# Performance work log

Measured on AMD Instinct MI355X. Metric: run time of the kernel, lower is better.

Reference implementation:

```python
import jax, jax.numpy as jnp
import numpy as np


def setup_inputs() -> dict:
    key = jax.random.key(0)
    k1, k2 = jax.random.split(key)
    B, N, C, H, W = 16, 10000, 3, 32, 32
    x = jax.random.normal(k1, (B, C, H, W), dtype=jnp.float32)
    images = jax.random.normal(k2, (N, C, H, W), dtype=jnp.float32)
    # sval = schedule(t) in (0,1); bt^2 = sval, at = sqrt(1 - sval)
    sval = jnp.asarray(0.5, dtype=jnp.float32)
    return {"x": x, "images": images, "sval": sval}


def reference(x, images, sval):
    # Original math: pwise = x[:,None] - at*images[None]
    #   weights = softmax(-||pwise||^2 / (2 bt^2), over N)
    #   out = -sum_n weights_n * pwise_n / bt^2
    # We decompose ||x - at*img||^2 = ||x||^2 - 2 at x.img + at^2 ||img||^2
    # (GEMM form) and use sum_n w_n (x - at*img_n) = x - at*(w @ imgs),
    # avoiding the [B,N,C,H,W] intermediate. Identical math.
    bt2 = sval                      # bt^2 = schedule(t)
    at = jnp.sqrt(1.0 - sval)       # at = sqrt(1 - schedule(t))
    B = x.shape[0]
    N = images.shape[0]
    xf = x.reshape(B, -1)           # [B, D]
    imf = images.reshape(N, -1)     # [N, D]
    x_sq = jnp.sum(xf * xf, axis=-1)        # [B]
    i_sq = jnp.sum(imf * imf, axis=-1)      # [N]
    cross = xf @ imf.T                      # [B, N]  (main GEMM)
    weight_args = -(x_sq[:, None] - 2.0 * at * cross
                    + (at * at) * i_sq[None, :]) / (2.0 * bt2)
    weights = jax.nn.softmax(weight_args, axis=1)   # [B, N]
    mix = weights @ imf                             # [B, D]
    out = -(xf - at * mix) / bt2                    # [B, D]
    return out.reshape(x.shape)
```

## Files before the change

kernel.cpp:

```cpp
#include <hip/hip_runtime.h>
#include <math.h>

#define BB 16
#define NN 10000
#define DD 3072
#define SEL_CUT 40.0f

#define RSTEP(mm, cc)                                              \
  {                                                                \
    const bool up = (lane & (mm)) != 0;                            \
    _Pragma("unroll")                                              \
    for (int k = 0; k < (cc); ++k) {                               \
      float lo = acc[k], hi = acc[k + (cc)];                       \
      float send = up ? lo : hi;                                   \
      float recv = __shfl_xor(send, (mm), 64);                     \
      acc[k] = (up ? hi : lo) + recv;                              \
    }                                                              \
  }

__global__ __launch_bounds__(256, 3) void k1_partial(
    const float* __restrict__ x, const float* __restrict__ images,
    const float* __restrict__ svalp, float* __restrict__ pd)
{
  const int t = threadIdx.x;
  const int lane = t & 63;
  const int wave = t >> 6;
  const int n0 = blockIdx.x * 16 + wave * 4;
  const int q = blockIdx.y;
  const int d0 = q * 768;

  float acc[64];
  float isq[4];
#pragma unroll
  for (int j = 0; j < 64; ++j) acc[j] = 0.f;
#pragma unroll
  for (int r = 0; r < 4; ++r) isq[r] = 0.f;

#pragma unroll 1
  for (int c = 0; c < 3; ++c) {
    const int dg = d0 + c * 256 + (lane << 2);
    float4 im[4];
#pragma unroll
    for (int r = 0; r < 4; ++r)
      im[r] = *(const float4*)&images[(size_t)(n0 + r) * DD + dg];
#pragma unroll
    for (int r = 0; r < 4; ++r)
      isq[r] += im[r].x * im[r].x + im[r].y * im[r].y +
                im[r].z * im[r].z + im[r].w * im[r].w;
#pragma unroll
    for (int b = 0; b < BB; ++b) {
      float4 xv = *(const float4*)&x[b * DD + dg];
#pragma unroll
      for (int r = 0; r < 4; ++r)
        acc[b * 4 + r] += im[r].x * xv.x + im[r].y * xv.y +
                          im[r].z * xv.z + im[r].w * xv.w;
    }
  }

  RSTEP(32, 32)
  RSTEP(16, 16)
  RSTEP(8, 8)
  RSTEP(4, 4)
  RSTEP(2, 2)
  RSTEP(1, 1)

#pragma unroll
  for (int r = 0; r < 4; ++r) {
    float v = isq[r];
#pragma unroll
    for (int m = 32; m >= 1; m >>= 1) v += __shfl_xor(v, m, 64);
    isq[r] = v;
  }

  const float sval = *svalp;
  const float at = sqrtf(1.f - sval);
  const float c1 = at / sval;
  const float c2 = (1.f - sval) / (2.f * sval);

  const int b = lane >> 2;
  const int r = lane & 3;
  float myisq = isq[0];
  if (r == 1) myisq = isq[1];
  if (r == 2) myisq = isq[2];
  if (r == 3) myisq = isq[3];

  pd[(size_t)b * NN * 4 + (size_t)(n0 + r) * 4 + q] = c1 * acc[0] - c2 * myisq;
}

__global__ __launch_bounds__(1024) void k2_select(
    const float* __restrict__ pd, int* __restrict__ cnt,
    int* __restrict__ idx, float* __restrict__ wv)
{
  __shared__ float red[16];
  __shared__ float mshared, lshared;
  const int b = blockIdx.x;
  const int t = threadIdx.x;
  const int lane = t & 63, wave = t >> 6;
  if (t == 0) cnt[b] = 0;

  float a[10];
#pragma unroll
  for (int i = 0; i < 10; ++i) {
    int n = t + (i << 10);
    if (n < NN) {
      float4 p = *(const float4*)&pd[(size_t)b * NN * 4 + (size_t)n * 4];
      a[i] = (p.x + p.y) + (p.z + p.w);
    } else {
      a[i] = -INFINITY;
    }
  }

  float mx = -INFINITY;
#pragma unroll
  for (int i = 0; i < 10; ++i) mx = fmaxf(mx, a[i]);
#pragma unroll
  for (int m = 32; m >= 1; m >>= 1) mx = fmaxf(mx, __shfl_xor(mx, m, 64));
  if (lane == 0) red[wave] = mx;
  __syncthreads();
  if (wave == 0) {
    float v = (lane < 16) ? red[lane] : -INFINITY;
#pragma unroll
    for (int m = 8; m >= 1; m >>= 1) v = fmaxf(v, __shfl_xor(v, m, 64));
    if (lane == 0) mshared = v;
  }
  __syncthreads();
  mx = mshared;

  float s = 0.f;
#pragma unroll
  for (int i = 0; i < 10; ++i) s += __expf(a[i] - mx);
#pragma unroll
  for (int m = 32; m >= 1; m >>= 1) s += __shfl_xor(s, m, 64);
  if (lane == 0) red[wave] = s;
  __syncthreads();
  if (wave == 0) {
    float v = (lane < 16) ? red[lane] : 0.f;
#pragma unroll
    for (int m = 8; m >= 1; m >>= 1) v += __shfl_xor(v, m, 64);
    if (lane == 0) lshared = v;
  }
  __syncthreads();
  const float invl = 1.f / lshared;

#pragma unroll
  for (int i = 0; i < 10; ++i) {
    if (a[i] > mx - SEL_CUT) {
      int k = atomicAdd(&cnt[b], 1);
      idx[b * NN + k] = t + (i << 10);
      wv[b * NN + k] = __expf(a[i] - mx) * invl;
    }
  }
}

__global__ __launch_bounds__(256) void k3_sparse(
    const float* __restrict__ images, const float* __restrict__ x,
    const float* __restrict__ svalp, const int* __restrict__ cnt,
    const int* __restrict__ idx, const float* __restrict__ wv,
    float* __restrict__ out)
{
  const int b = blockIdx.y;
  const int d0 = blockIdx.x * 1024 + (threadIdx.x << 2);
  const int c = cnt[b];

  float4 acc = make_float4(0.f, 0.f, 0.f, 0.f);
  for (int j = 0; j < c; ++j) {
    int n = idx[b * NN + j];
    float w = wv[b * NN + j];
    float4 im = *(const float4*)&images[(size_t)n * DD + d0];
    acc.x += w * im.x; acc.y += w * im.y;
    acc.z += w * im.z; acc.w += w * im.w;
  }

  const float sval = *svalp;
  const float at = sqrtf(1.f - sval);
  const float inv_bt2 = 1.f / sval;
  float4 xv = *(const float4*)&x[b * DD + d0];
  float4 o;
  o.x = (at * acc.x - xv.x) * inv_bt2;
  o.y = (at * acc.y - xv.y) * inv_bt2;
  o.z = (at * acc.z - xv.z) * inv_bt2;
  o.w = (at * acc.w - xv.w) * inv_bt2;
  *(float4*)&out[b * DD + d0] = o;
}

extern "C" void kernel_launch(void* const* d_in, const int* in_sizes, int n_in,
                              void* d_out, int out_size, void* d_ws, size_t ws_size,
                              hipStream_t stream) {
  const float* x      = (const float*)d_in[0];
  const float* images = (const float*)d_in[1];
  const float* sval   = (const float*)d_in[2];
  float* out = (float*)d_out;
  float* ws  = (float*)d_ws;

  float* pd  = ws;
  int*   cnt = (int*)(ws + 640000);
  int*   idx = (int*)(ws + 640032);
  float* wv  = ws + 800032;

  hipLaunchKernelGGL(k1_partial, dim3(625, 4), dim3(256), 0, stream,
                     x, images, sval, pd);
  hipLaunchKernelGGL(k2_select, dim3(16), dim3(1024), 0, stream,
                     pd, cnt, idx, wv);
  hipLaunchKernelGGL(k3_sparse, dim3(3, 16), dim3(256), 0, stream,
                     images, x, sval, cnt, idx, wv, out);
}
```

Baseline: 235.9 us.

## Keep x slice in registers and stream image pairs with finer D split

The partial-dot kernel now splits D into 12 chunks of 256 and holds the 16 x vectors for its chunk in registers. Each wave loops over 16 images two at a time, prefetching the next pair and reducing the pair dot products with a two-wide shuffle transpose. The partial-sum layout moves to [q][b][n], so the select kernel sums 12 strided partials, and the selected-candidate buffers are capped at 1024 per batch row. The aim is to cut repeated x reloads and the 64-register accumulator, at the cost of more partial writes and reads and more shuffles per image.

```diff
diff --git a/kernel.cpp b/kernel.cpp
--- a/kernel.cpp
+++ b/kernel.cpp
@@ -4,87 +4,100 @@
 #define BB 16
 #define NN 10000
 #define DD 3072
+#define QQ 12
 #define SEL_CUT 40.0f
-
-#define RSTEP(mm, cc)                                              \
-  {                                                                \
-    const bool up = (lane & (mm)) != 0;                            \
-    _Pragma("unroll")                                              \
-    for (int k = 0; k < (cc); ++k) {                               \
-      float lo = acc[k], hi = acc[k + (cc)];                       \
-      float send = up ? lo : hi;                                   \
-      float recv = __shfl_xor(send, (mm), 64);                     \
-      acc[k] = (up ? hi : lo) + recv;                              \
-    }                                                              \
-  }
-
-__global__ __launch_bounds__(256, 3) void k1_partial(
+#define CAP 1024
+
+#define RSTEP2(mm, cc)                                                  \
+  {                                                                     \
+    const bool up = (lane & (mm)) != 0;                                 \
+    _Pragma("unroll")                                                   \
+    for (int k = 0; k < (cc); ++k) {                                    \
+      float2 lo = accp[k], hi = accp[k + (cc)];                         \
+      float sx = up ? lo.x : hi.x, sy = up ? lo.y : hi.y;               \
+      float rx = __shfl_xor(sx, (mm), 64);                              \
+      float ry = __shfl_xor(sy, (mm), 64);                              \
+      accp[k].x = (up ? hi.x : lo.x) + rx;                              \
+      accp[k].y = (up ? hi.y : lo.y) + ry;                              \
+    }                                                                   \
+  }
+
+__global__ __launch_bounds__(256) void k1_partial(
     const float* __restrict__ x, const float* __restrict__ images,
     const float* __restrict__ svalp, float* __restrict__ pd)
 {
   const int t = threadIdx.x;
   const int lane = t & 63;
   const int wave = t >> 6;
-  const int n0 = blockIdx.x * 16 + wave * 4;
   const int q = blockIdx.y;
-  const int d0 = q * 768;
-
-  float acc[64];
-  float isq[4];
-#pragma unroll
-  for (int j = 0; j < 64; ++j) acc[j] = 0.f;
-#pragma unroll
-  for (int r = 0; r < 4; ++r) isq[r] = 0.f;
-
-#pragma unroll 1
-  for (int c = 0; c < 3; ++c) {
-    const int dg = d0 + c * 256 + (lane << 2);
-    float4 im[4];
-#pragma unroll
-    for (int r = 0; r < 4; ++r)
-      im[r] = *(const float4*)&images[(size_t)(n0 + r) * DD + dg];
-#pragma unroll
-    for (int r = 0; r < 4; ++r)
-      isq[r] += im[r].x * im[r].x + im[r].y * im[r].y +
-                im[r].z * im[r].z + im[r].w * im[r].w;
-#pragma unroll
-    for (int b = 0; b < BB; ++b) {
-      float4 xv = *(const float4*)&x[b * DD + dg];
-#pragma unroll
-      for (int r = 0; r < 4; ++r)
-        acc[b * 4 + r] += im[r].x * xv.x + im[r].y * xv.y +
-                          im[r].z * xv.z + im[r].w * xv.w;
-    }
-  }
-
-  RSTEP(32, 32)
-  RSTEP(16, 16)
-  RSTEP(8, 8)
-  RSTEP(4, 4)
-  RSTEP(2, 2)
-  RSTEP(1, 1)
-
-#pragma unroll
-  for (int r = 0; r < 4; ++r) {
-    float v = isq[r];
-#pragma unroll
-    for (int m = 32; m >= 1; m >>= 1) v += __shfl_xor(v, m, 64);
-    isq[r] = v;
-  }
+  const int dg = q * 256 + (lane << 2);
+  const int n0 = (blockIdx.x * 4 + wave) * 16;
+
+  float4 xr[BB];
+#pragma unroll
+  for (int b = 0; b < BB; ++b)
+    xr[b] = *(const float4*)&x[b * DD + dg];
 
   const float sval = *svalp;
   const float at = sqrtf(1.f - sval);
-  const float c1 = at / sval;
-  const float c2 = (1.f - sval) / (2.f * sval);
-
-  const int b = lane >> 2;
-  const int r = lane & 3;
-  float myisq = isq[0];
-  if (r == 1) myisq = isq[1];
-  if (r == 2) myisq = isq[2];
-  if (r == 3) myisq = isq[3];
-
-  pd[(size_t)b * NN * 4 + (size_t)(n0 + r) * 4 + q] = c1 * acc[0] - c2 * myisq;
+  const float k1c = at / sval;
+  const float k2c = (1.f - sval) / (2.f * sval);
+
+  int n = n0;
+  float4 A0 = *(const float4*)&images[(size_t)(n < NN ? n : NN - 1) * DD + dg];
+  float4 A1 = *(const float4*)&images[(size_t)(n + 1 < NN ? n + 1 : NN - 1) * DD + dg];
+
+#pragma unroll 1
+  for (int g = 0; g < 8; ++g) {
+    float2 p0 = make_float2(A0.x, A1.x);
+    float2 p1 = make_float2(A0.y, A1.y);
+    float2 p2 = make_float2(A0.z, A1.z);
+    float2 p3 = make_float2(A0.w, A1.w);
+
+    const int n2 = n + 2;
+    if (g != 7) {
+      A0 = *(const float4*)&images[(size_t)(n2 < NN ? n2 : NN - 1) * DD + dg];
+      A1 = *(const float4*)&images[(size_t)(n2 + 1 < NN ? n2 + 1 : NN - 1) * DD + dg];
+    }
+
+    float2 isqp;
+    isqp.x = p0.x * p0.x + p1.x * p1.x + p2.x * p2.x + p3.x * p3.x;
+    isqp.y = p0.y * p0.y + p1.y * p1.y + p2.y * p2.y + p3.y * p3.y;
+
+    float2 accp[BB];
+#pragma unroll
+    for (int b = 0; b < BB; ++b) {
+      accp[b].x = p0.x * xr[b].x + p1.x * xr[b].y +
+                  p2.x * xr[b].z + p3.x * xr[b].w;
+      accp[b].y = p0.y * xr[b].x + p1.y * xr[b].y +
+                  p2.y * xr[b].z + p3.y * xr[b].w;
+    }
+
+    RSTEP2(32, 8)
+    RSTEP2(16, 4)
+    RSTEP2(8, 2)
+    RSTEP2(4, 1)
+    accp[0].x += __shfl_xor(accp[0].x, 2, 64);
+    accp[0].y += __shfl_xor(accp[0].y, 2, 64);
+    accp[0].x += __shfl_xor(accp[0].x, 1, 64);
+    accp[0].y += __shfl_xor(accp[0].y, 1, 64);
+
+#pragma unroll
+    for (int m = 32; m >= 1; m >>= 1) {
+      isqp.x += __shfl_xor(isqp.x, m, 64);
+      isqp.y += __shfl_xor(isqp.y, m, 64);
+    }
+
+    const int r = lane & 1;
+    const int bb = (lane >> 2) & 15;
+    const int nn = n + r;
+    float dotv = r ? accp[0].y : accp[0].x;
+    float isv  = r ? isqp.y    : isqp.x;
+    if ((lane & 2) == 0 && nn < NN)
+      pd[((size_t)q * BB + bb) * NN + nn] = k1c * dotv - k2c * isv;
+
+    n = n2;
+  }
 }
 
 __global__ __launch_bounds__(1024) void k2_select(
@@ -103,8 +116,11 @@
   for (int i = 0; i < 10; ++i) {
     int n = t + (i << 10);
     if (n < NN) {
-      float4 p = *(const float4*)&pd[(size_t)b * NN * 4 + (size_t)n * 4];
-      a[i] = (p.x + p.y) + (p.z + p.w);
+      float s = 0.f;
+#pragma unroll
+      for (int qq = 0; qq < QQ; ++qq)
+        s += pd[((size_t)qq * BB + b) * NN + n];
+      a[i] = s;
     } else {
       a[i] = -INFINITY;
     }
@@ -146,8 +162,10 @@
   for (int i = 0; i < 10; ++i) {
     if (a[i] > mx - SEL_CUT) {
       int k = atomicAdd(&cnt[b], 1);
-      idx[b * NN + k] = t + (i << 10);
-      wv[b * NN + k] = __expf(a[i] - mx) * invl;
+      if (k < CAP) {
+        idx[b * CAP + k] = t + (i << 10);
+        wv[b * CAP + k] = __expf(a[i] - mx) * invl;
+      }
     }
   }
 }
@@ -160,12 +178,13 @@
 {
   const int b = blockIdx.y;
   const int d0 = blockIdx.x * 1024 + (threadIdx.x << 2);
-  const int c = cnt[b];
+  int c = cnt[b];
+  if (c > CAP) c = CAP;
 
   float4 acc = make_float4(0.f, 0.f, 0.f, 0.f);
   for (int j = 0; j < c; ++j) {
-    int n = idx[b * NN + j];
-    float w = wv[b * NN + j];
+    int n = idx[b * CAP + j];
+    float w = wv[b * CAP + j];
     float4 im = *(const float4*)&images[(size_t)n * DD + d0];
     acc.x += w * im.x; acc.y += w * im.y;
     acc.z += w * im.z; acc.w += w * im.w;
@@ -193,11 +212,11 @@
   float* ws  = (float*)d_ws;
 
   float* pd  = ws;
-  int*   cnt = (int*)(ws + 640000);
-  int*   idx = (int*)(ws + 640032);
-  float* wv  = ws + 800032;
-
-  hipLaunchKernelGGL(k1_partial, dim3(625, 4), dim3(256), 0, stream,
+  int*   cnt = (int*)(ws + 1920000);
+  int*   idx = (int*)(ws + 1920032);
+  float* wv  = ws + 1936416;
+
+  hipLaunchKernelGGL(k1_partial, dim3(157, QQ), dim3(256), 0, stream,
                      x, images, sval, pd);
   hipLaunchKernelGGL(k2_select, dim3(16), dim3(1024), 0, stream,
                      pd, cnt, idx, wv);
```

After: 211.3 us. 1.12x faster.
